# Kernel optimization log

Measured on AMD Instinct MI355X. Metric: run time of the kernel, lower is better.

Reference implementation:

```python
import jax, jax.numpy as jnp
import numpy as np

N_NODES = 50000
N_EDGES = 800000
IN_DIM = 128
HID = 128
BN_EPS = 1e-5


def setup_inputs() -> dict:
    key = jax.random.key(0)
    ks = jax.random.split(key, 8)
    x = jax.random.normal(ks[0], (N_NODES, IN_DIM), dtype=jnp.float32)
    edge_index = jax.random.randint(ks[1], (2, N_EDGES), 0, N_NODES, dtype=jnp.int64)
    s1 = 1.0 / np.sqrt(IN_DIM)
    s2 = 1.0 / np.sqrt(HID)
    return {
        'x': x,
        'edge_index': edge_index,
        'w1_0': jax.random.normal(ks[2], (IN_DIM, HID), dtype=jnp.float32) * s1,
        'b1_0': jnp.zeros((HID,), dtype=jnp.float32),
        'w2_0': jax.random.normal(ks[3], (HID, HID), dtype=jnp.float32) * s2,
        'b2_0': jnp.zeros((HID,), dtype=jnp.float32),
        'g_0': jnp.ones((HID,), dtype=jnp.float32),
        'be_0': jnp.zeros((HID,), dtype=jnp.float32),
        'w1_1': jax.random.normal(ks[4], (HID, HID), dtype=jnp.float32) * s2,
        'b1_1': jnp.zeros((HID,), dtype=jnp.float32),
        'w2_1': jax.random.normal(ks[5], (HID, HID), dtype=jnp.float32) * s2,
        'b2_1': jnp.zeros((HID,), dtype=jnp.float32),
        'g_1': jnp.ones((HID,), dtype=jnp.float32),
        'be_1': jnp.zeros((HID,), dtype=jnp.float32),
    }


def _gin_layer(h, src, dst, w1, b1, w2, b2, g, be):
    # GINConv with eps=0: MLP(h_i + sum_{j->i} h_j); scatter-add over targets
    agg = jax.ops.segment_sum(h[src], dst, num_segments=N_NODES)
    z = h + agg
    z = jax.nn.relu(z @ w1 + b1) @ w2 + b2
    # BatchNorm1d (training mode: batch stats over nodes, biased variance)
    mu = jnp.mean(z, axis=0)
    var = jnp.mean(jnp.square(z - mu), axis=0)
    z = (z - mu) * jax.lax.rsqrt(var + BN_EPS) * g + be
    return jax.nn.relu(z)


def reference(x, edge_index, w1_0, b1_0, w2_0, b2_0, g_0, be_0,
              w1_1, b1_1, w2_1, b2_1, g_1, be_1):
    src, dst = edge_index[0], edge_index[1]
    h = _gin_layer(x, src, dst, w1_0, b1_0, w2_0, b2_0, g_0, be_0)
    # dropout p=0.0 -> no-op between layers
    h = _gin_layer(h, src, dst, w1_1, b1_1, w2_1, b2_1, g_1, be_1)
    return h
```

## Files before the change

### kernel.cpp

```cpp
#include <hip/hip_runtime.h>
#include <hip/hip_bf16.h>

#define HID 128
#define LDA 136
#define CAP 64

typedef __attribute__((ext_vector_type(8))) short frag8;
typedef __attribute__((ext_vector_type(4))) float f32x4;

__device__ inline float bf2f(unsigned short u) {
    return __uint_as_float(((unsigned int)u) << 16);
}
__device__ inline unsigned short f2bf(float f) {
    __hip_bfloat16 h = __float2bfloat16(f);
    return __builtin_bit_cast(unsigned short, h);
}
__device__ inline float4 u4tof4(ushort4 u) {
    return make_float4(bf2f(u.x), bf2f(u.y), bf2f(u.z), bf2f(u.w));
}
__device__ inline ushort4 f4tou4(float4 f) {
    ushort4 u; u.x = f2bf(f.x); u.y = f2bf(f.y); u.z = f2bf(f.z); u.w = f2bf(f.w);
    return u;
}
__device__ inline float4 bnrelu4(float4 u, float4 s, float4 b) {
    float4 r;
    r.x = fmaxf(fmaf(u.x, s.x, b.x), 0.0f);
    r.y = fmaxf(fmaf(u.y, s.y, b.y), 0.0f);
    r.z = fmaxf(fmaf(u.z, s.z, b.z), 0.0f);
    r.w = fmaxf(fmaf(u.w, s.w, b.w), 0.0f);
    return r;
}
__device__ inline void acc4(float4& a, float4 u) {
    a.x += u.x; a.y += u.y; a.z += u.z; a.w += u.w;
}

__global__ __launch_bounds__(256) void prep_k(
    const float* __restrict__ x, unsigned short* __restrict__ B0,
    const float* __restrict__ w0, const float* __restrict__ w1,
    const float* __restrict__ w2, const float* __restrict__ w3,
    unsigned short* __restrict__ wt,
    int* __restrict__ zbase, int zcount4,
    long total4, int vb, int zblocks)
{
    int bid = blockIdx.x;
    int t = threadIdx.x;
    if (bid < vb) {
        long i = bid * 256L + t;
        if (i < total4)
            ((ushort4*)B0)[i] = f4tou4(((const float4*)x)[i]);
    } else if (bid < vb + 4) {
        int w_id = bid - vb;
        const float* w = (w_id == 0) ? w0 : (w_id == 1) ? w1 : (w_id == 2) ? w2 : w3;
        unsigned short* o = wt + (size_t)w_id * 128 * 128;
        for (int i = 0; i < 64; i++) {
            int idx = t + i * 256;
            int k = idx >> 7, nn = idx & 127;
            o[nn * 128 + k] = f2bf(w[idx]);
        }
    } else {
        int zb = bid - vb - 4;
        int4 zero = make_int4(0, 0, 0, 0);
        for (int i = zb * 256 + t; i < zcount4; i += zblocks * 256)
            ((int4*)zbase)[i] = zero;
    }
}

__global__ __launch_bounds__(256) void fill_k(
    const int* __restrict__ src, const int* __restrict__ dst,
    int* __restrict__ cursor, int* __restrict__ eidx, int n_edges, int half)
{
    int gid = blockIdx.x * 256 + threadIdx.x;
    if (gid < half) {
        int d = dst[gid];
        int p = atomicAdd(&cursor[d], 1);
        if (p < CAP) eidx[d * CAP + p] = src[gid];
    }
    int e1 = gid + half;
    if (e1 < n_edges) {
        int d = dst[e1];
        int p = atomicAdd(&cursor[d], 1);
        if (p < CAP) eidx[d * CAP + p] = src[e1];
    }
}

template<bool BN>
__global__ __launch_bounds__(256) void gather_t(
    const unsigned short* __restrict__ h, unsigned short* __restrict__ z,
    const int* __restrict__ cnt, const int* __restrict__ eidx,
    const float* __restrict__ S, const float* __restrict__ g,
    const float* __restrict__ be, float inv_n, int n)
{
    __shared__ float lsc[BN ? 128 : 1], lsh[BN ? 128 : 1];
    if (BN) {
        int t = threadIdx.x;
        if (t < 128) {
            float mu = S[t] * inv_n;
            float var = fmaf(-mu, mu, S[128 + t] * inv_n);
            float s = g[t] * rsqrtf(var + 1e-5f);
            lsc[t] = s;
            lsh[t] = fmaf(-mu, s, be[t]);
        }
        __syncthreads();
    }

    int tid = blockIdx.x * 256 + threadIdx.x;
    int v = tid >> 5;
    if (v >= n) return;
    int q = (tid & 31) << 2;

    float4 scv, shv;
    if (BN) {
        scv = *(const float4*)(lsc + q);
        shv = *(const float4*)(lsh + q);
    }

    float4 a0 = u4tof4(*(const ushort4*)(h + (size_t)v * HID + q));
    if (BN) a0 = bnrelu4(a0, scv, shv);
    float4 a1 = make_float4(0.f, 0.f, 0.f, 0.f);

    const int* bucket = eidx + (size_t)v * CAP;
    int deg = cnt[v];
    if (deg > CAP) deg = CAP;

    int i = 0;
    for (; i + 4 <= deg; i += 4) {
        int s0 = bucket[i + 0];
        int s1 = bucket[i + 1];
        int s2 = bucket[i + 2];
        int s3 = bucket[i + 3];
        float4 u0 = u4tof4(*(const ushort4*)(h + (size_t)s0 * HID + q));
        float4 u1 = u4tof4(*(const ushort4*)(h + (size_t)s1 * HID + q));
        float4 u2 = u4tof4(*(const ushort4*)(h + (size_t)s2 * HID + q));
        float4 u3 = u4tof4(*(const ushort4*)(h + (size_t)s3 * HID + q));
        if (BN) {
            u0 = bnrelu4(u0, scv, shv);
            u1 = bnrelu4(u1, scv, shv);
            u2 = bnrelu4(u2, scv, shv);
            u3 = bnrelu4(u3, scv, shv);
        }
        acc4(a0, u0); acc4(a1, u1); acc4(a0, u2); acc4(a1, u3);
    }
    for (; i < deg; i++) {
        float4 u = u4tof4(*(const ushort4*)(h + (size_t)bucket[i] * HID + q));
        if (BN) u = bnrelu4(u, scv, shv);
        acc4(a0, u);
    }
    acc4(a0, a1);
    *(ushort4*)(z + (size_t)v * HID + q) = f4tou4(a0);
}

template<bool RELU, bool STATS>
__global__ __launch_bounds__(256) void mfma_gemm(
    const unsigned short* __restrict__ Z, const unsigned short* __restrict__ Wt,
    const float* __restrict__ bias, unsigned short* __restrict__ out,
    float* __restrict__ S, int n_rows)
{
    __shared__ unsigned short Ws[128 * LDA];
    __shared__ float red[STATS ? 1024 : 1];

    const int t = threadIdx.x;
    const int row0 = blockIdx.x * 128;

    {
        const int chunk = t & 15;
        const int rbase = t >> 4;
        #pragma unroll
        for (int it = 0; it < 8; it++) {
            int r = rbase + it * 16;
            *(uint4*)(Ws + r * LDA + chunk * 8) =
                *(const uint4*)(Wt + (size_t)r * HID + chunk * 8);
        }
    }
    __syncthreads();

    const int wave = t >> 6;
    const int lane = t & 63;
    const int l15  = lane & 15;
    const int quad = lane >> 4;

    const int r0 = row0 + wave * 32 + l15;
    const int r1 = r0 + 16;
    const int rs0 = (r0 < n_rows) ? r0 : 0;
    const int rs1 = (r1 < n_rows) ? r1 : 0;
    frag8 a0[4], a1[4];
    #pragma unroll
    for (int kk = 0; kk < 4; kk++) {
        a0[kk] = *(const frag8*)(Z + (size_t)rs0 * HID + kk * 32 + quad * 8);
        a1[kk] = *(const frag8*)(Z + (size_t)rs1 * HID + kk * 32 + quad * 8);
    }

    f32x4 acc[2][8];
    #pragma unroll
    for (int tr = 0; tr < 2; tr++)
        #pragma unroll
        for (int tc = 0; tc < 8; tc++)
            acc[tr][tc] = (f32x4){0.f, 0.f, 0.f, 0.f};

    #pragma unroll
    for (int kk = 0; kk < 4; kk++) {
        int ko = kk * 32 + quad * 8;
        #pragma unroll
        for (int tc = 0; tc < 8; tc++) {
            frag8 b = *(const frag8*)(Ws + (tc * 16 + l15) * LDA + ko);
            acc[0][tc] = __builtin_amdgcn_mfma_f32_16x16x32_bf16(a0[kk], b, acc[0][tc], 0, 0, 0);
            acc[1][tc] = __builtin_amdgcn_mfma_f32_16x16x32_bf16(a1[kk], b, acc[1][tc], 0, 0, 0);
        }
    }

    const int wrow = row0 + wave * 32;
    #pragma unroll
    for (int tc = 0; tc < 8; tc++) {
        const int col = tc * 16 + l15;
        const float bc = bias[col];
        float s = 0.f, sq = 0.f;
        #pragma unroll
        for (int tr = 0; tr < 2; tr++) {
            #pragma unroll
            for (int r = 0; r < 4; r++) {
                int grow = wrow + tr * 16 + quad * 4 + r;
                float o = acc[tr][tc][r] + bc;
                if (grow < n_rows) {
                    if (STATS) { s += o; sq = fmaf(o, o, sq); }
                    if (RELU) o = fmaxf(o, 0.f);
                    out[(size_t)grow * HID + col] = f2bf(o);
                }
            }
        }
        if (STATS) {
            s  += __shfl_xor(s, 16);  s  += __shfl_xor(s, 32);
            sq += __shfl_xor(sq, 16); sq += __shfl_xor(sq, 32);
            if (lane < 16) {
                red[wave * 128 + col] = s;
                red[512 + wave * 128 + col] = sq;
            }
        }
    }
    if (STATS) {
        __syncthreads();
        int which = t >> 7, c = t & 127;
        const float* rp = red + which * 512;
        atomicAdd(&S[which * 128 + c],
                  rp[c] + rp[128 + c] + rp[256 + c] + rp[384 + c]);
    }
}

__global__ __launch_bounds__(256) void bn_apply_f32_k(
    const unsigned short* __restrict__ z, const float* __restrict__ S,
    const float* __restrict__ g, const float* __restrict__ be,
    float* __restrict__ out, float inv_n, long total4)
{
    __shared__ float lsc[128], lsh[128];
    int t = threadIdx.x;
    if (t < 128) {
        float mu = S[t] * inv_n;
        float var = fmaf(-mu, mu, S[128 + t] * inv_n);
        float s = g[t] * rsqrtf(var + 1e-5f);
        lsc[t] = s;
        lsh[t] = fmaf(-mu, s, be[t]);
    }
    __syncthreads();

    long i = blockIdx.x * 256L + t;
    if (i >= total4) return;
    float4 v = u4tof4(((const ushort4*)z)[i]);
    int c0 = ((int)(i & 31)) * 4;
    v.x = fmaxf(fmaf(v.x, lsc[c0 + 0], lsh[c0 + 0]), 0.0f);
    v.y = fmaxf(fmaf(v.y, lsc[c0 + 1], lsh[c0 + 1]), 0.0f);
    v.z = fmaxf(fmaf(v.z, lsc[c0 + 2], lsh[c0 + 2]), 0.0f);
    v.w = fmaxf(fmaf(v.w, lsc[c0 + 3], lsh[c0 + 3]), 0.0f);
    ((float4*)out)[i] = v;
}

extern "C" void kernel_launch(void* const* d_in, const int* in_sizes, int n_in,
                              void* d_out, int out_size, void* d_ws, size_t ws_size,
                              hipStream_t stream)
{
    const float* x    = (const float*)d_in[0];
    const int*   ei   = (const int*)d_in[1];
    const float* w1_0 = (const float*)d_in[2];
    const float* b1_0 = (const float*)d_in[3];
    const float* w2_0 = (const float*)d_in[4];
    const float* b2_0 = (const float*)d_in[5];
    const float* g_0  = (const float*)d_in[6];
    const float* be_0 = (const float*)d_in[7];
    const float* w1_1 = (const float*)d_in[8];
    const float* b1_1 = (const float*)d_in[9];
    const float* w2_1 = (const float*)d_in[10];
    const float* b2_1 = (const float*)d_in[11];
    const float* g_1  = (const float*)d_in[12];
    const float* be_1 = (const float*)d_in[13];
    float* OUT = (float*)d_out;

    const int n       = in_sizes[0] / HID;
    const int n_edges = in_sizes[1] / 2;
    const int* src = ei;
    const int* dst = ei + n_edges;
    const float inv_n = 1.0f / (float)n;

    char* p = (char*)d_ws;
    unsigned short* B0 = (unsigned short*)p;  p += (size_t)n * HID * sizeof(short);
    unsigned short* B1 = (unsigned short*)p;  p += (size_t)n * HID * sizeof(short);
    unsigned short* Wt = (unsigned short*)p;  p += (size_t)4 * 128 * 128 * sizeof(short);
    int*   cursor = (int*)p;    p += (size_t)n * sizeof(int);
    float* S0     = (float*)p;  p += 256 * sizeof(float);
    float* S1     = (float*)p;  p += 256 * sizeof(float);
    int*   eidx   = (int*)p;    p += (size_t)n * CAP * sizeof(int);

    unsigned short* B2 = (unsigned short*)d_out;

    dim3 blk(256);
    const long total4 = (long)n * (HID / 4);
    const int vb = (int)((total4 + 255) / 256);
    const int zblocks = 32;
    const int zcount4 = (n + 512 + 3) / 4;
    const int half = (n_edges + 1) / 2;
    const int fb = (half + 255) / 256;
    const int gb = (n * 32 + 255) / 256;
    const int gemm_blocks = (n + 127) / 128;

    prep_k<<<vb + 4 + zblocks, blk, 0, stream>>>(
        x, B0, w1_0, w2_0, w1_1, w2_1, Wt, cursor, zcount4, total4, vb, zblocks);
    fill_k<<<fb, blk, 0, stream>>>(src, dst, cursor, eidx, n_edges, half);

    gather_t<false><<<gb, blk, 0, stream>>>(B0, B1, cursor, eidx,
                                            nullptr, nullptr, nullptr, inv_n, n);
    mfma_gemm<true,  false><<<gemm_blocks, blk, 0, stream>>>(B1, Wt,             b1_0, B2, nullptr, n);
    mfma_gemm<false, true ><<<gemm_blocks, blk, 0, stream>>>(B2, Wt + 16384,     b2_0, B0, S0, n);

    gather_t<true><<<gb, blk, 0, stream>>>(B0, B1, cursor, eidx,
                                           S0, g_0, be_0, inv_n, n);
    mfma_gemm<true,  false><<<gemm_blocks, blk, 0, stream>>>(B1, Wt + 2 * 16384, b1_1, B2, nullptr, n);
    mfma_gemm<false, true ><<<gemm_blocks, blk, 0, stream>>>(B2, Wt + 3 * 16384, b2_1, B1, S1, n);
    bn_apply_f32_k<<<vb, blk, 0, stream>>>(B1, S1, g_1, be_1, OUT, inv_n, total4);
}
```

Measured before the change: 322.4 us.

## Fuse two-layer MLP GEMMs with LDS intermediate and merge prep/fill kernels

Replaces the two separate MFMA GEMM launches per GIN layer with one kernel that keeps the ReLU hidden activations in shared memory and feeds them into the second GEMM, avoiding a global round trip of the intermediate. The edge bucket fill is merged into the prep kernel, and cursor/stat zeroing moves to hipMemsetAsync. The gather loop gains an 8-way unrolled path for more memory-level parallelism. Weight fragments are now read directly from global memory rather than staged in LDS, which may add cache pressure.

```diff
diff --git a/kernel.cpp b/kernel.cpp
--- a/kernel.cpp
+++ b/kernel.cpp
@@ -34,22 +34,30 @@
     a.x += u.x; a.y += u.y; a.z += u.z; a.w += u.w;
 }
 
-__global__ __launch_bounds__(256) void prep_k(
+__global__ __launch_bounds__(256) void mega_prep_k(
     const float* __restrict__ x, unsigned short* __restrict__ B0,
     const float* __restrict__ w0, const float* __restrict__ w1,
     const float* __restrict__ w2, const float* __restrict__ w3,
     unsigned short* __restrict__ wt,
-    int* __restrict__ zbase, int zcount4,
-    long total4, int vb, int zblocks)
-{
-    int bid = blockIdx.x;
-    int t = threadIdx.x;
-    if (bid < vb) {
-        long i = bid * 256L + t;
+    const int* __restrict__ src, const int* __restrict__ dst,
+    int* __restrict__ cursor, int* __restrict__ eidx,
+    int n_edges, long total4, int fb, int vb)
+{
+    const int bid = blockIdx.x;
+    const int t = threadIdx.x;
+    if (bid < fb) {
+        int e = bid * 256 + t;
+        if (e < n_edges) {
+            int d = dst[e];
+            int p = atomicAdd(&cursor[d], 1);
+            if (p < CAP) eidx[d * CAP + p] = src[e];
+        }
+    } else if (bid < fb + vb) {
+        long i = (long)(bid - fb) * 256 + t;
         if (i < total4)
             ((ushort4*)B0)[i] = f4tou4(((const float4*)x)[i]);
-    } else if (bid < vb + 4) {
-        int w_id = bid - vb;
+    } else {
+        int w_id = bid - fb - vb;
         const float* w = (w_id == 0) ? w0 : (w_id == 1) ? w1 : (w_id == 2) ? w2 : w3;
         unsigned short* o = wt + (size_t)w_id * 128 * 128;
         for (int i = 0; i < 64; i++) {
@@ -57,29 +65,6 @@
             int k = idx >> 7, nn = idx & 127;
             o[nn * 128 + k] = f2bf(w[idx]);
         }
-    } else {
-        int zb = bid - vb - 4;
-        int4 zero = make_int4(0, 0, 0, 0);
-        for (int i = zb * 256 + t; i < zcount4; i += zblocks * 256)
-            ((int4*)zbase)[i] = zero;
-    }
-}
-
-__global__ __launch_bounds__(256) void fill_k(
-    const int* __restrict__ src, const int* __restrict__ dst,
-    int* __restrict__ cursor, int* __restrict__ eidx, int n_edges, int half)
-{
-    int gid = blockIdx.x * 256 + threadIdx.x;
-    if (gid < half) {
-        int d = dst[gid];
-        int p = atomicAdd(&cursor[d], 1);
-        if (p < CAP) eidx[d * CAP + p] = src[gid];
-    }
-    int e1 = gid + half;
-    if (e1 < n_edges) {
-        int d = dst[e1];
-        int p = atomicAdd(&cursor[d], 1);
-        if (p < CAP) eidx[d * CAP + p] = src[e1];
     }
 }
 
@@ -123,20 +108,38 @@
     if (deg > CAP) deg = CAP;
 
     int i = 0;
+    for (; i + 8 <= deg; i += 8) {
+        int s0 = bucket[i + 0], s1 = bucket[i + 1];
+        int s2 = bucket[i + 2], s3 = bucket[i + 3];
+        int s4 = bucket[i + 4], s5 = bucket[i + 5];
+        int s6 = bucket[i + 6], s7 = bucket[i + 7];
+        float4 u0 = u4tof4(*(const ushort4*)(h + (size_t)s0 * HID + q));
+        float4 u1 = u4tof4(*(const ushort4*)(h + (size_t)s1 * HID + q));
+        float4 u2 = u4tof4(*(const ushort4*)(h + (size_t)s2 * HID + q));
+        float4 u3 = u4tof4(*(const ushort4*)(h + (size_t)s3 * HID + q));
+        float4 u4 = u4tof4(*(const ushort4*)(h + (size_t)s4 * HID + q));
+        float4 u5 = u4tof4(*(const ushort4*)(h + (size_t)s5 * HID + q));
+        float4 u6 = u4tof4(*(const ushort4*)(h + (size_t)s6 * HID + q));
+        float4 u7 = u4tof4(*(const ushort4*)(h + (size_t)s7 * HID + q));
+        if (BN) {
+            u0 = bnrelu4(u0, scv, shv); u1 = bnrelu4(u1, scv, shv);
+            u2 = bnrelu4(u2, scv, shv); u3 = bnrelu4(u3, scv, shv);
+            u4 = bnrelu4(u4, scv, shv); u5 = bnrelu4(u5, scv, shv);
+            u6 = bnrelu4(u6, scv, shv); u7 = bnrelu4(u7, scv, shv);
+        }
+        acc4(a0, u0); acc4(a1, u1); acc4(a0, u2); acc4(a1, u3);
+        acc4(a0, u4); acc4(a1, u5); acc4(a0, u6); acc4(a1, u7);
+    }
     for (; i + 4 <= deg; i += 4) {
-        int s0 = bucket[i + 0];
-        int s1 = bucket[i + 1];
-        int s2 = bucket[i + 2];
-        int s3 = bucket[i + 3];
+        int s0 = bucket[i + 0], s1 = bucket[i + 1];
+        int s2 = bucket[i + 2], s3 = bucket[i + 3];
         float4 u0 = u4tof4(*(const ushort4*)(h + (size_t)s0 * HID + q));
         float4 u1 = u4tof4(*(const ushort4*)(h + (size_t)s1 * HID + q));
         float4 u2 = u4tof4(*(const ushort4*)(h + (size_t)s2 * HID + q));
         float4 u3 = u4tof4(*(const ushort4*)(h + (size_t)s3 * HID + q));
         if (BN) {
-            u0 = bnrelu4(u0, scv, shv);
-            u1 = bnrelu4(u1, scv, shv);
-            u2 = bnrelu4(u2, scv, shv);
-            u3 = bnrelu4(u3, scv, shv);
+            u0 = bnrelu4(u0, scv, shv); u1 = bnrelu4(u1, scv, shv);
+            u2 = bnrelu4(u2, scv, shv); u3 = bnrelu4(u3, scv, shv);
         }
         acc4(a0, u0); acc4(a1, u1); acc4(a0, u2); acc4(a1, u3);
     }
@@ -149,30 +152,17 @@
     *(ushort4*)(z + (size_t)v * HID + q) = f4tou4(a0);
 }
 
-template<bool RELU, bool STATS>
-__global__ __launch_bounds__(256) void mfma_gemm(
-    const unsigned short* __restrict__ Z, const unsigned short* __restrict__ Wt,
-    const float* __restrict__ bias, unsigned short* __restrict__ out,
+__global__ __launch_bounds__(256) void mlp_k(
+    unsigned short* __restrict__ Z,
+    const unsigned short* __restrict__ W1t, const float* __restrict__ b1,
+    const unsigned short* __restrict__ W2t, const float* __restrict__ b2,
     float* __restrict__ S, int n_rows)
 {
-    __shared__ unsigned short Ws[128 * LDA];
-    __shared__ float red[STATS ? 1024 : 1];
+    __shared__ unsigned short Hs[128 * LDA];
+    __shared__ float red[1024];
 
     const int t = threadIdx.x;
     const int row0 = blockIdx.x * 128;
-
-    {
-        const int chunk = t & 15;
-        const int rbase = t >> 4;
-        #pragma unroll
-        for (int it = 0; it < 8; it++) {
-            int r = rbase + it * 16;
-            *(uint4*)(Ws + r * LDA + chunk * 8) =
-                *(const uint4*)(Wt + (size_t)r * HID + chunk * 8);
-        }
-    }
-    __syncthreads();
-
     const int wave = t >> 6;
     const int lane = t & 63;
     const int l15  = lane & 15;
@@ -201,42 +191,76 @@
         int ko = kk * 32 + quad * 8;
         #pragma unroll
         for (int tc = 0; tc < 8; tc++) {
-            frag8 b = *(const frag8*)(Ws + (tc * 16 + l15) * LDA + ko);
+            frag8 b = *(const frag8*)(W1t + (size_t)(tc * 16 + l15) * HID + ko);
             acc[0][tc] = __builtin_amdgcn_mfma_f32_16x16x32_bf16(a0[kk], b, acc[0][tc], 0, 0, 0);
             acc[1][tc] = __builtin_amdgcn_mfma_f32_16x16x32_bf16(a1[kk], b, acc[1][tc], 0, 0, 0);
         }
     }
 
-    const int wrow = row0 + wave * 32;
+    const int wrow = wave * 32;
     #pragma unroll
     for (int tc = 0; tc < 8; tc++) {
         const int col = tc * 16 + l15;
-        const float bc = bias[col];
-        float s = 0.f, sq = 0.f;
+        const float bc = b1[col];
         #pragma unroll
         for (int tr = 0; tr < 2; tr++) {
             #pragma unroll
             for (int r = 0; r < 4; r++) {
-                int grow = wrow + tr * 16 + quad * 4 + r;
+                int lrow = wrow + tr * 16 + quad * 4 + r;
+                Hs[lrow * LDA + col] = f2bf(fmaxf(acc[tr][tc][r] + bc, 0.f));
+            }
+        }
+    }
+    __syncthreads();
+
+    #pragma unroll
+    for (int kk = 0; kk < 4; kk++) {
+        a0[kk] = *(const frag8*)(Hs + (wave * 32 + l15) * LDA + kk * 32 + quad * 8);
+        a1[kk] = *(const frag8*)(Hs + (wave * 32 + 16 + l15) * LDA + kk * 32 + quad * 8);
+    }
+    #pragma unroll
+    for (int tr = 0; tr < 2; tr++)
+        #pragma unroll
+        for (int tc = 0; tc < 8; tc++)
+            acc[tr][tc] = (f32x4){0.f, 0.f, 0.f, 0.f};
+
+    #pragma unroll
+    for (int kk = 0; kk < 4; kk++) {
+        int ko = kk * 32 + quad * 8;
+        #pragma unroll
+        for (int tc = 0; tc < 8; tc++) {
+            frag8 b = *(const frag8*)(W2t + (size_t)(tc * 16 + l15) * HID + ko);
+            acc[0][tc] = __builtin_amdgcn_mfma_f32_16x16x32_bf16(a0[kk], b, acc[0][tc], 0, 0, 0);
+            acc[1][tc] = __builtin_amdgcn_mfma_f32_16x16x32_bf16(a1[kk], b, acc[1][tc], 0, 0, 0);
+        }
+    }
+
+    #pragma unroll
+    for (int tc = 0; tc < 8; tc++) {
+        const int col = tc * 16 + l15;
+        const float bc = b2[col];
+        float s = 0.f, sq = 0.f;
+        #pragma unroll
+        for (int tr = 0; tr < 2; tr++) {
+            #pragma unroll
+            for (int r = 0; r < 4; r++) {
+                int grow = row0 + wrow + tr * 16 + quad * 4 + r;
                 float o = acc[tr][tc][r] + bc;
                 if (grow < n_rows) {
-                    if (STATS) { s += o; sq = fmaf(o, o, sq); }
-                    if (RELU) o = fmaxf(o, 0.f);
-                    out[(size_t)grow * HID + col] = f2bf(o);
+                    s += o; sq = fmaf(o, o, sq);
+                    Z[(size_t)grow * HID + col] = f2bf(o);
                 }
             }
         }
-        if (STATS) {
-            s  += __shfl_xor(s, 16);  s  += __shfl_xor(s, 32);
-            sq += __shfl_xor(sq, 16); sq += __shfl_xor(sq, 32);
-            if (lane < 16) {
-                red[wave * 128 + col] = s;
-                red[512 + wave * 128 + col] = sq;
-            }
-        }
-    }
-    if (STATS) {
-        __syncthreads();
+        s  += __shfl_xor(s, 16);  s  += __shfl_xor(s, 32);
+        sq += __shfl_xor(sq, 16); sq += __shfl_xor(sq, 32);
+        if (lane < 16) {
+            red[wave * 128 + col] = s;
+            red[512 + wave * 128 + col] = sq;
+        }
+    }
+    __syncthreads();
+    {
         int which = t >> 7, c = t & 127;
         const float* rp = red + which * 512;
         atomicAdd(&S[which * 128 + c],
@@ -306,30 +330,25 @@
     float* S1     = (float*)p;  p += 256 * sizeof(float);
     int*   eidx   = (int*)p;    p += (size_t)n * CAP * sizeof(int);
 
-    unsigned short* B2 = (unsigned short*)d_out;
-
     dim3 blk(256);
     const long total4 = (long)n * (HID / 4);
     const int vb = (int)((total4 + 255) / 256);
-    const int zblocks = 32;
-    const int zcount4 = (n + 512 + 3) / 4;
-    const int half = (n_edges + 1) / 2;
-    const int fb = (half + 255) / 256;
+    const int fb = (n_edges + 255) / 256;
     const int gb = (n * 32 + 255) / 256;
-    const int gemm_blocks = (n + 127) / 128;
-
-    prep_k<<<vb + 4 + zblocks, blk, 0, stream>>>(
-        x, B0, w1_0, w2_0, w1_1, w2_1, Wt, cursor, zcount4, total4, vb, zblocks);
-    fill_k<<<fb, blk, 0, stream>>>(src, dst, cursor, eidx, n_edges, half);
+    const int mlp_blocks = (n + 127) / 128;
+
+    hipMemsetAsync(cursor, 0, (size_t)n * sizeof(int) + 512 * sizeof(float), stream);
+    mega_prep_k<<<fb + vb + 4, blk, 0, stream>>>(
+        x, B0, w1_0, w2_0, w1_1, w2_1, Wt, src, dst, cursor, eidx,
+        n_edges, total4, fb, vb);
 
     gather_t<false><<<gb, blk, 0, stream>>>(B0, B1, cursor, eidx,
                                             nullptr, nullptr, nullptr, inv_n, n);
-    mfma_gemm<true,  false><<<gemm_blocks, blk, 0, stream>>>(B1, Wt,             b1_0, B2, nullptr, n);
-    mfma_gemm<false, true ><<<gemm_blocks, blk, 0, stream>>>(B2, Wt + 16384,     b2_0, B0, S0, n);
-
-    gather_t<true><<<gb, blk, 0, stream>>>(B0, B1, cursor, eidx,
+    mlp_k<<<mlp_blocks, blk, 0, stream>>>(B1, Wt, b1_0, Wt + 16384, b2_0, S0, n);
+
+    gather_t<true><<<gb, blk, 0, stream>>>(B1, B0, cursor, eidx,
                                            S0, g_0, be_0, inv_n, n);
-    mfma_gemm<true,  false><<<gemm_blocks, blk, 0, stream>>>(B1, Wt + 2 * 16384, b1_1, B2, nullptr, n);
-    mfma_gemm<false, true ><<<gemm_blocks, blk, 0, stream>>>(B2, Wt + 3 * 16384, b2_1, B1, S1, n);
-    bn_apply_f32_k<<<vb, blk, 0, stream>>>(B1, S1, g_1, be_1, OUT, inv_n, total4);
-}
+    mlp_k<<<mlp_blocks, blk, 0, stream>>>(B0, Wt + 2 * 16384, b1_1,
+                                          Wt + 3 * 16384, b2_1, S1, n);
+    bn_apply_f32_k<<<vb, blk, 0, stream>>>(B0, S1, g_1, be_1, OUT, inv_n, total4);
+}
```

New measurement: 293.9 us. 1.1x faster.
